# Kernel optimization log

Measured on AMD Instinct MI355X. Metric: run time of the kernel, lower is better.

## Reference

```python
import jax, jax.numpy as jnp
import numpy as np

IN_F, H, T, NUM_CLASSES, WINDOW_HALF = 14, 24, 25, 4, 12


def _lstm_dir(x_tbf, w_ih, w_hh, b_ih, b_hh, reverse):
    # x_tbf: [T,B,F]; w_ih: [4H,F]; w_hh: [4H,H]; biases: [4H]
    B = x_tbf.shape[1]
    xw = jnp.einsum('tbf,gf->tbg', x_tbf, w_ih) + b_ih + b_hh  # [T,B,4H]

    def step(carry, xw_t):
        h, c = carry
        gates = xw_t + h @ w_hh.T
        i, f, g, o = jnp.split(gates, 4, axis=-1)
        i, f, o = jax.nn.sigmoid(i), jax.nn.sigmoid(f), jax.nn.sigmoid(o)
        g = jnp.tanh(g)
        c = f * c + i * g
        h = o * jnp.tanh(c)
        return (h, c), h

    h0 = jnp.zeros((B, H), x_tbf.dtype)
    c0 = jnp.zeros((B, H), x_tbf.dtype)
    _, hs = jax.lax.scan(step, (h0, c0), xw, reverse=reverse)
    return hs  # [T,B,H], in original time order


def setup_inputs() -> dict:
    key = jax.random.key(0)
    ks = jax.random.split(key, 12)
    s_ih = 1.0 / np.sqrt(H)
    u = lambda k, shape: jax.random.uniform(k, shape, jnp.float32, -s_ih, s_ih)
    return {
        'x': jax.random.normal(ks[0], (65536, T, IN_F), jnp.float32),
        'w_ih_f': u(ks[1], (4 * H, IN_F)),
        'w_hh_f': u(ks[2], (4 * H, H)),
        'b_ih_f': u(ks[3], (4 * H,)),
        'b_hh_f': u(ks[4], (4 * H,)),
        'w_ih_b': u(ks[5], (4 * H, IN_F)),
        'w_hh_b': u(ks[6], (4 * H, H)),
        'b_ih_b': u(ks[7], (4 * H,)),
        'b_hh_b': u(ks[8], (4 * H,)),
        'head_w': u(ks[9], (NUM_CLASSES, 2 * H)),
        'head_b': u(ks[10], (NUM_CLASSES,)),
    }


def reference(x, w_ih_f, w_hh_f, b_ih_f, b_hh_f, w_ih_b, w_hh_b, b_ih_b, b_hh_b, head_w, head_b):
    x_tbf = jnp.transpose(x, (1, 0, 2))  # [T,B,F]
    h_f = _lstm_dir(x_tbf, w_ih_f, w_hh_f, b_ih_f, b_hh_f, reverse=False)
    h_b = _lstm_dir(x_tbf, w_ih_b, w_hh_b, b_ih_b, b_hh_b, reverse=True)
    center = jnp.concatenate([h_f[WINDOW_HALF], h_b[WINDOW_HALF]], axis=-1)  # [B,2H]
    # dropout is identity in eval mode
    return center @ head_w.T + head_b  # [B,4]
```

## Files before the change

### kernel.cpp

```cpp
#include <hip/hip_runtime.h>

typedef __attribute__((ext_vector_type(8))) short frag8;
typedef __attribute__((ext_vector_type(4))) float f4;
typedef __attribute__((ext_vector_type(4))) unsigned int u4;
typedef __attribute__((ext_vector_type(2))) float f2;

namespace {
constexpr int T_STEPS = 25;
constexpr int IN_F    = 14;
constexpr int H       = 24;
constexpr int NSTEP   = 13;
constexpr int XSLOTS  = 7;
constexpr int LDS_HOFF = 14336;
constexpr float LOG2E  = 1.4426950408889634f;
constexpr float TWOLOG2E = 2.8853900817779268f;
}

#if __has_builtin(__builtin_amdgcn_exp2f)
#define EXP2F(v) __builtin_amdgcn_exp2f(v)
#else
#define EXP2F(v) __expf(0.6931471805599453f * (v))
#endif

__device__ __forceinline__ unsigned short bf16_rne(float f) {
    unsigned int u = __float_as_uint(f);
    u += 0x7fff + ((u >> 16) & 1);
    return (unsigned short)(u >> 16);
}
__device__ __forceinline__ float bf16_to_f(unsigned short s) {
    return __uint_as_float(((unsigned int)s) << 16);
}
__device__ __forceinline__ float fast_rcp(float x) { return __builtin_amdgcn_rcpf(x); }

__global__ void pack_mfma(const float* __restrict__ wif, const float* __restrict__ whf,
                          const float* __restrict__ bif, const float* __restrict__ bhf,
                          const float* __restrict__ wib, const float* __restrict__ whb,
                          const float* __restrict__ bib, const float* __restrict__ bhb,
                          unsigned short* __restrict__ ws)
{
    const int gid = blockIdx.x * 256 + threadIdx.x;
    if (gid >= 2048) return;
    const int lane = gid & 63;
    const int tile = (gid >> 6) & 7;
    const int set  = (gid >> 9) & 1;
    const int dir  = (gid >> 10) & 1;
    const int n = lane & 15, q = lane >> 4;
    const int r = tile * 16 + n;
    const int g = r >> 5, u_row = r & 31;
    const bool vrow = (u_row < 24);
    const float* Wx = dir ? wib : wif;
    const float* Wh = dir ? whb : whf;
    const float* bi = dir ? bib : bif;
    const float* bh = dir ? bhb : bhf;
    const int rowW = g * 24 + (vrow ? u_row : 0);
    const float scale = (g == 2) ? TWOLOG2E : -LOG2E;
    unsigned short vals[8];
    #pragma unroll
    for (int j = 0; j < 8; ++j) {
        const int k = q * 8 + j;
        unsigned short o = 0;
        if (vrow) {
            if (set == 0) {
                if (k < 28) {
                    const int f = (k < 14) ? k : k - 14;
                    o = bf16_rne(scale * Wx[rowW * IN_F + f]);
                } else if (k < 30) {
                    const float b = scale * (bi[rowW] + bh[rowW]);
                    const unsigned short hi = bf16_rne(b);
                    o = (k == 28) ? hi : bf16_rne(b - bf16_to_f(hi));
                }
            } else {
                const int uh = (k & 1) ? (k >> 1) + 16 : (k >> 1);
                if (uh < 24) o = bf16_rne(scale * Wh[rowW * H + uh]);
            }
        }
        vals[j] = o;
    }
    unsigned short* d = ws + (size_t)gid * 8;
    #pragma unroll
    for (int j = 0; j < 8; ++j) d[j] = vals[j];
}

__global__ __launch_bounds__(128, 3)
void bilstm_mfma(const float* __restrict__ x, const unsigned short* __restrict__ wpk,
                 const float* __restrict__ head_w, const float* __restrict__ head_b,
                 float* __restrict__ out, int B)
{
    __align__(16) __shared__ unsigned char arena[19456];

    const int tid  = threadIdx.x;
    const int wave = __builtin_amdgcn_readfirstlane(tid >> 6);
    const int lane = tid & 63;
    const int q    = lane >> 4;
    const int col  = lane & 15;
    const int b0   = blockIdx.x * 16;

    frag8 Bf[2][8];
    #pragma unroll
    for (int s = 0; s < 2; ++s)
        #pragma unroll
        for (int t = 0; t < 8; ++t)
            Bf[s][t] = ((const frag8*)wpk)[((wave * 2 + s) * 8 + t) * 64 + lane];

    unsigned char* xbase = arena + wave * (XSLOTS * 1024);
    unsigned char* hbase = arena + LDS_HOFF + wave * 2560;

    auto stage_x = [&](int si, int e, int step) {
        const int t = wave ? (T_STEPS - 1 - step) : step;
        const float* xr = x + ((size_t)(b0 + e) * T_STEPS + t) * IN_F;
        unsigned int xu[IN_F];
        #pragma unroll
        for (int i = 0; i < 7; ++i) {
            f2 v = *(const f2*)(xr + 2 * i);
            xu[2*i] = __float_as_uint(v.x); xu[2*i+1] = __float_as_uint(v.y);
        }
        unsigned int lo[IN_F];
        #pragma unroll
        for (int i = 0; i < IN_F; ++i)
            lo[i] = __float_as_uint(__uint_as_float(xu[i])
                                    - __uint_as_float(xu[i] & 0xFFFF0000u));
        unsigned int w[16];
        #pragma unroll
        for (int i = 0; i < 7; ++i)
            w[i] = __builtin_amdgcn_perm(xu[2*i+1], xu[2*i], 0x07060302u);
        w[7] = __builtin_amdgcn_perm(lo[1], lo[0], 0x07060302u);
        #pragma unroll
        for (int i = 0; i < 6; ++i)
            w[8 + i] = __builtin_amdgcn_perm(lo[2*i+3], lo[2*i+2], 0x07060302u);
        w[14] = 0x3F803F80u;
        w[15] = 0u;
        #pragma unroll
        for (int qq = 0; qq < 4; ++qq)
            *(u4*)(xbase + si * 1024 + qq * 256 + e * 16) =
                (u4){w[qq*4], w[qq*4+1], w[qq*4+2], w[qq*4+3]};
    };

    for (int rr = lane; rr < XSLOTS * 16; rr += 64) stage_x(rr >> 4, rr & 15, rr >> 4);

    float c_st[2][4];
    #pragma unroll
    for (int p = 0; p < 2; ++p)
        #pragma unroll
        for (int r = 0; r < 4; ++r) c_st[p][r] = 0.0f;

    const unsigned char* xrd = xbase + q * 256 + col * 16;
    const unsigned char* hrd = hbase + col * 80 + q * 16;
    unsigned char* hwr = hbase + col * 4;

    auto gates_and_store = [&](f4* acc) {
        #pragma unroll
        for (int r = 0; r < 4; ++r) {
            float hv[2], hl[2];
            #pragma unroll
            for (int p = 0; p < 2; ++p) {
                const float ig = fast_rcp(1.0f + EXP2F(acc[0 + p][r]));
                const float fg = fast_rcp(1.0f + EXP2F(acc[2 + p][r]));
                const float gg = 1.0f - 2.0f * fast_rcp(1.0f + EXP2F(acc[4 + p][r]));
                const float og = fast_rcp(1.0f + EXP2F(acc[6 + p][r]));
                const float cn = fg * c_st[p][r] + ig * gg;
                c_st[p][r] = cn;
                const float tc = 1.0f - 2.0f * fast_rcp(1.0f + EXP2F(TWOLOG2E * cn));
                const float h  = og * tc;
                const float hh = __uint_as_float(__float_as_uint(h) & 0xFFFF0000u);
                hv[p] = h;
                hl[p] = h - hh;
            }
            const unsigned int whi = __builtin_amdgcn_perm(
                __float_as_uint(hv[1]), __float_as_uint(hv[0]), 0x07060302u);
            const unsigned int wlo = __builtin_amdgcn_perm(
                __float_as_uint(hl[1]), __float_as_uint(hl[0]), 0x07060302u);
            *(unsigned int*)(hwr + (q * 4 + r) * 80)        = whi;
            *(unsigned int*)(hwr + (q * 4 + r) * 80 + 1280) = wlo;
        }
    };

    {
        const frag8 Ax = *(const frag8*)(xrd);
        f4 acc[8];
        #pragma unroll
        for (int t = 0; t < 8; ++t) acc[t] = (f4){0.f, 0.f, 0.f, 0.f};
        #pragma unroll
        for (int t = 0; t < 8; ++t)
            acc[t] = __builtin_amdgcn_mfma_f32_16x16x32_bf16(Ax, Bf[0][t], acc[t], 0, 0, 0);
        gates_and_store(acc);
    }

    #pragma unroll 1
    for (int s = 1; s < NSTEP; ++s) {
        if (s == XSLOTS) {
            for (int rr = lane; rr < (NSTEP - XSLOTS) * 16; rr += 64)
                stage_x(rr >> 4, rr & 15, XSLOTS + (rr >> 4));
        }
        const int xs = (s < XSLOTS) ? s : s - XSLOTS;
        const frag8 Ax  = *(const frag8*)(xrd + xs * 1024);
        const frag8 Ahh = *(const frag8*)(hrd);
        const frag8 Ahl = *(const frag8*)(hrd + 1280);

        f4 acc[8];
        #pragma unroll
        for (int t = 0; t < 8; ++t) acc[t] = (f4){0.f, 0.f, 0.f, 0.f};
        #pragma unroll
        for (int t = 0; t < 8; ++t) {
            acc[t] = __builtin_amdgcn_mfma_f32_16x16x32_bf16(Ax,  Bf[0][t], acc[t], 0, 0, 0);
            acc[t] = __builtin_amdgcn_mfma_f32_16x16x32_bf16(Ahh, Bf[1][t], acc[t], 0, 0, 0);
            acc[t] = __builtin_amdgcn_mfma_f32_16x16x32_bf16(Ahl, Bf[1][t], acc[t], 0, 0, 0);
        }
        gates_and_store(acc);
    }

    __syncthreads();

    if (tid < 64) {
        const int e = tid >> 2, cls = tid & 3;
        float acc = head_b[cls];
        #pragma unroll
        for (int u = 0; u < H; ++u) {
            const int so = 2 * ((u & 15) * 2 + (u >> 4));
            const unsigned char* hf0 = arena + LDS_HOFF + e * 80 + so;
            const float hf = bf16_to_f(*(const unsigned short*)(hf0))
                           + bf16_to_f(*(const unsigned short*)(hf0 + 1280));
            const float hb = bf16_to_f(*(const unsigned short*)(hf0 + 2560))
                           + bf16_to_f(*(const unsigned short*)(hf0 + 2560 + 1280));
            acc += hf * head_w[cls * 2 * H + u] + hb * head_w[cls * 2 * H + H + u];
        }
        out[(size_t)b0 * 4 + tid] = acc;
    }
}

extern "C" void kernel_launch(void* const* d_in, const int* in_sizes, int n_in,
                              void* d_out, int out_size, void* d_ws, size_t ws_size,
                              hipStream_t stream)
{
    const float* x      = (const float*)d_in[0];
    const float* w_ih_f = (const float*)d_in[1];
    const float* w_hh_f = (const float*)d_in[2];
    const float* b_ih_f = (const float*)d_in[3];
    const float* b_hh_f = (const float*)d_in[4];
    const float* w_ih_b = (const float*)d_in[5];
    const float* w_hh_b = (const float*)d_in[6];
    const float* b_ih_b = (const float*)d_in[7];
    const float* b_hh_b = (const float*)d_in[8];
    const float* head_w = (const float*)d_in[9];
    const float* head_b = (const float*)d_in[10];
    float* out = (float*)d_out;
    unsigned short* ws = (unsigned short*)d_ws;

    const int B = in_sizes[0] / (T_STEPS * IN_F);

    hipLaunchKernelGGL(pack_mfma, dim3(8), dim3(256), 0, stream,
                       w_ih_f, w_hh_f, b_ih_f, b_hh_f,
                       w_ih_b, w_hh_b, b_ih_b, b_hh_b, ws);
    hipLaunchKernelGGL(bilstm_mfma, dim3((B + 15) / 16), dim3(128), 0, stream,
                       x, ws, head_w, head_b, out, B);
}
```

Baseline: 201.6 us.

## Swap MFMA operand roles to keep hidden state in registers, stage all x upfront

```diff
diff --git a/kernel.cpp b/kernel.cpp
--- a/kernel.cpp
+++ b/kernel.cpp
@@ -10,9 +10,8 @@
 constexpr int IN_F    = 14;
 constexpr int H       = 24;
 constexpr int NSTEP   = 13;
-constexpr int XSLOTS  = 7;
-constexpr int LDS_HOFF = 14336;
-constexpr float LOG2E  = 1.4426950408889634f;
+constexpr int WAVE_LDS = NSTEP * 1024;
+constexpr float LOG2E    = 1.4426950408889634f;
 constexpr float TWOLOG2E = 2.8853900817779268f;
 }
 
@@ -70,7 +69,8 @@
                     o = (k == 28) ? hi : bf16_rne(b - bf16_to_f(hi));
                 }
             } else {
-                const int uh = (k & 1) ? (k >> 1) + 16 : (k >> 1);
+                const int j7 = k & 7, kq = k >> 3;
+                const int uh = (j7 < 4) ? kq * 4 + j7 : 16 + kq * 4 + (j7 - 4);
                 if (uh < 24) o = bf16_rne(scale * Wh[rowW * H + uh]);
             }
         }
@@ -86,7 +86,7 @@
                  const float* __restrict__ head_w, const float* __restrict__ head_b,
                  float* __restrict__ out, int B)
 {
-    __align__(16) __shared__ unsigned char arena[19456];
+    __align__(16) __shared__ unsigned char arena[2 * WAVE_LDS];
 
     const int tid  = threadIdx.x;
     const int wave = __builtin_amdgcn_readfirstlane(tid >> 6);
@@ -95,18 +95,17 @@
     const int col  = lane & 15;
     const int b0   = blockIdx.x * 16;
 
-    frag8 Bf[2][8];
+    frag8 Aw[2][8];
     #pragma unroll
     for (int s = 0; s < 2; ++s)
         #pragma unroll
         for (int t = 0; t < 8; ++t)
-            Bf[s][t] = ((const frag8*)wpk)[((wave * 2 + s) * 8 + t) * 64 + lane];
-
-    unsigned char* xbase = arena + wave * (XSLOTS * 1024);
-    unsigned char* hbase = arena + LDS_HOFF + wave * 2560;
-
-    auto stage_x = [&](int si, int e, int step) {
-        const int t = wave ? (T_STEPS - 1 - step) : step;
+            Aw[s][t] = ((const frag8*)wpk)[((wave * 2 + s) * 8 + t) * 64 + lane];
+
+    unsigned char* xbase = arena + wave * WAVE_LDS;
+
+    auto stage_x = [&](int si, int e) {
+        const int t = wave ? (T_STEPS - 1 - si) : si;
         const float* xr = x + ((size_t)(b0 + e) * T_STEPS + t) * IN_F;
         unsigned int xu[IN_F];
         #pragma unroll
@@ -135,7 +134,7 @@
                 (u4){w[qq*4], w[qq*4+1], w[qq*4+2], w[qq*4+3]};
     };
 
-    for (int rr = lane; rr < XSLOTS * 16; rr += 64) stage_x(rr >> 4, rr & 15, rr >> 4);
+    for (int rr = lane; rr < NSTEP * 16; rr += 64) stage_x(rr >> 4, rr & 15);
 
     float c_st[2][4];
     #pragma unroll
@@ -143,16 +142,18 @@
         #pragma unroll
         for (int r = 0; r < 4; ++r) c_st[p][r] = 0.0f;
 
+    float hv[2][4];
+    frag8 Bhh, Bhl;
+    const f4 zc = {0.f, 0.f, 0.f, 0.f};
+
     const unsigned char* xrd = xbase + q * 256 + col * 16;
-    const unsigned char* hrd = hbase + col * 80 + q * 16;
-    unsigned char* hwr = hbase + col * 4;
-
-    auto gates_and_store = [&](f4* acc) {
-        #pragma unroll
-        for (int r = 0; r < 4; ++r) {
-            float hv[2], hl[2];
+
+    auto gates = [&](f4* acc) {
+        float hl[2][4];
+        #pragma unroll
+        for (int p = 0; p < 2; ++p) {
             #pragma unroll
-            for (int p = 0; p < 2; ++p) {
+            for (int r = 0; r < 4; ++r) {
                 const float ig = fast_rcp(1.0f + EXP2F(acc[0 + p][r]));
                 const float fg = fast_rcp(1.0f + EXP2F(acc[2 + p][r]));
                 const float gg = 1.0f - 2.0f * fast_rcp(1.0f + EXP2F(acc[4 + p][r]));
@@ -161,68 +162,60 @@
                 c_st[p][r] = cn;
                 const float tc = 1.0f - 2.0f * fast_rcp(1.0f + EXP2F(TWOLOG2E * cn));
                 const float h  = og * tc;
-                const float hh = __uint_as_float(__float_as_uint(h) & 0xFFFF0000u);
-                hv[p] = h;
-                hl[p] = h - hh;
+                hv[p][r] = h;
+                hl[p][r] = h - __uint_as_float(__float_as_uint(h) & 0xFFFF0000u);
             }
-            const unsigned int whi = __builtin_amdgcn_perm(
-                __float_as_uint(hv[1]), __float_as_uint(hv[0]), 0x07060302u);
-            const unsigned int wlo = __builtin_amdgcn_perm(
-                __float_as_uint(hl[1]), __float_as_uint(hl[0]), 0x07060302u);
-            *(unsigned int*)(hwr + (q * 4 + r) * 80)        = whi;
-            *(unsigned int*)(hwr + (q * 4 + r) * 80 + 1280) = wlo;
-        }
+        }
+        const u4 uh4 = {
+            __builtin_amdgcn_perm(__float_as_uint(hv[0][1]), __float_as_uint(hv[0][0]), 0x07060302u),
+            __builtin_amdgcn_perm(__float_as_uint(hv[0][3]), __float_as_uint(hv[0][2]), 0x07060302u),
+            __builtin_amdgcn_perm(__float_as_uint(hv[1][1]), __float_as_uint(hv[1][0]), 0x07060302u),
+            __builtin_amdgcn_perm(__float_as_uint(hv[1][3]), __float_as_uint(hv[1][2]), 0x07060302u)};
+        const u4 ul4 = {
+            __builtin_amdgcn_perm(__float_as_uint(hl[0][1]), __float_as_uint(hl[0][0]), 0x07060302u),
+            __builtin_amdgcn_perm(__float_as_uint(hl[0][3]), __float_as_uint(hl[0][2]), 0x07060302u),
+            __builtin_amdgcn_perm(__float_as_uint(hl[1][1]), __float_as_uint(hl[1][0]), 0x07060302u),
+            __builtin_amdgcn_perm(__float_as_uint(hl[1][3]), __float_as_uint(hl[1][2]), 0x07060302u)};
+        Bhh = __builtin_bit_cast(frag8, uh4);
+        Bhl = __builtin_bit_cast(frag8, ul4);
     };
 
     {
-        const frag8 Ax = *(const frag8*)(xrd);
+        const frag8 Bx = *(const frag8*)(xrd);
         f4 acc[8];
         #pragma unroll
-        for (int t = 0; t < 8; ++t) acc[t] = (f4){0.f, 0.f, 0.f, 0.f};
-        #pragma unroll
         for (int t = 0; t < 8; ++t)
-            acc[t] = __builtin_amdgcn_mfma_f32_16x16x32_bf16(Ax, Bf[0][t], acc[t], 0, 0, 0);
-        gates_and_store(acc);
+            acc[t] = __builtin_amdgcn_mfma_f32_16x16x32_bf16(Aw[0][t], Bx, zc, 0, 0, 0);
+        gates(acc);
     }
 
     #pragma unroll 1
     for (int s = 1; s < NSTEP; ++s) {
-        if (s == XSLOTS) {
-            for (int rr = lane; rr < (NSTEP - XSLOTS) * 16; rr += 64)
-                stage_x(rr >> 4, rr & 15, XSLOTS + (rr >> 4));
-        }
-        const int xs = (s < XSLOTS) ? s : s - XSLOTS;
-        const frag8 Ax  = *(const frag8*)(xrd + xs * 1024);
-        const frag8 Ahh = *(const frag8*)(hrd);
-        const frag8 Ahl = *(const frag8*)(hrd + 1280);
-
+        const frag8 Bx = *(const frag8*)(xrd + s * 1024);
         f4 acc[8];
         #pragma unroll
-        for (int t = 0; t < 8; ++t) acc[t] = (f4){0.f, 0.f, 0.f, 0.f};
-        #pragma unroll
         for (int t = 0; t < 8; ++t) {
-            acc[t] = __builtin_amdgcn_mfma_f32_16x16x32_bf16(Ax,  Bf[0][t], acc[t], 0, 0, 0);
-            acc[t] = __builtin_amdgcn_mfma_f32_16x16x32_bf16(Ahh, Bf[1][t], acc[t], 0, 0, 0);
-            acc[t] = __builtin_amdgcn_mfma_f32_16x16x32_bf16(Ahl, Bf[1][t], acc[t], 0, 0, 0);
-        }
-        gates_and_store(acc);
-    }
+            acc[t] = __builtin_amdgcn_mfma_f32_16x16x32_bf16(Aw[0][t], Bx,  zc,     0, 0, 0);
+            acc[t] = __builtin_amdgcn_mfma_f32_16x16x32_bf16(Aw[1][t], Bhh, acc[t], 0, 0, 0);
+            acc[t] = __builtin_amdgcn_mfma_f32_16x16x32_bf16(Aw[1][t], Bhl, acc[t], 0, 0, 0);
+        }
+        gates(acc);
+    }
+
+    *(f4*)(xbase + col * 96 + q * 16) = (f4){hv[0][0], hv[0][1], hv[0][2], hv[0][3]};
+    if (q < 2)
+        *(f4*)(xbase + col * 96 + 64 + q * 16) = (f4){hv[1][0], hv[1][1], hv[1][2], hv[1][3]};
 
     __syncthreads();
 
     if (tid < 64) {
         const int e = tid >> 2, cls = tid & 3;
         float acc = head_b[cls];
-        #pragma unroll
-        for (int u = 0; u < H; ++u) {
-            const int so = 2 * ((u & 15) * 2 + (u >> 4));
-            const unsigned char* hf0 = arena + LDS_HOFF + e * 80 + so;
-            const float hf = bf16_to_f(*(const unsigned short*)(hf0))
-                           + bf16_to_f(*(const unsigned short*)(hf0 + 1280));
-            const float hb = bf16_to_f(*(const unsigned short*)(hf0 + 2560))
-                           + bf16_to_f(*(const unsigned short*)(hf0 + 2560 + 1280));
-            acc += hf * head_w[cls * 2 * H + u] + hb * head_w[cls * 2 * H + H + u];
-        }
+        const float* hf = (const float*)(arena + e * 96);
+        const float* hb = (const float*)(arena + WAVE_LDS + e * 96);
+        #pragma unroll
+        for (int u = 0; u < H; ++u)
+            acc += hf[u] * head_w[cls * 2 * H + u] + hb[u] * head_w[cls * 2 * H + H + u];
         out[(size_t)b0 * 4 + tid] = acc;
     }
 }
```

After: 198.0 us. No clear change (-1.8%).
